# Optimization experiments

Hardware: AMD Instinct MI355X
Metric: run time of the kernel (lower is better)

## Reference

```python
import jax, jax.numpy as jnp
import numpy as np

DIM = 512
HID = 2048
E = 16
B = 8
N = 2048
THRESHOLD = 0.8
CAP_FACTOR = 2.0  # eval mode
MIN_EXPERT_CAPACITY = 4
LOSS_COEF = 0.01
CAP = max(MIN_EXPERT_CAPACITY, min(N, int(N * CAP_FACTOR / E)))  # 256


def setup_inputs() -> dict:
    key = jax.random.key(0)
    k1, k2, k3, k4 = jax.random.split(key, 4)
    x = jax.random.normal(k1, (B, N, DIM), dtype=jnp.float32)
    w_gating = jax.random.normal(k2, (DIM, E), dtype=jnp.float32)
    std1 = 1.0 / np.sqrt(HID)
    std2 = 1.0 / np.sqrt(DIM)
    w1 = jax.random.uniform(k3, (E, DIM, HID), jnp.float32, -std1, std1)
    w2 = jax.random.uniform(k4, (E, HID, DIM), jnp.float32, -std2, std2)
    return {"x": x, "w_gating": w_gating, "w1": w1, "w2": w2}


def _gate(x, w_gating):
    # raw gate probabilities [B, N, E]
    raw = jax.nn.softmax(jnp.einsum('bnd,de->bne', x, w_gating), axis=-1)
    order = jnp.argsort(-raw, axis=-1)                      # descending sort indices
    sp = jnp.take_along_axis(raw, order, axis=-1)           # sorted probs (desc)
    cum = jnp.cumsum(sp, axis=-1)
    tm = cum >= THRESHOLD
    k = jnp.argmax(tm.astype(jnp.float32), axis=-1) + 1     # dynamic k per token
    k = jnp.where(jnp.any(tm, axis=-1), k, E)
    # select top-k in sorted order, renormalize
    rank = jnp.arange(E)
    sel = (rank < k[..., None]).astype(raw.dtype)           # [B,N,E] sorted order
    selp = sp * sel
    normp = selp / jnp.sum(selp, axis=-1, keepdims=True)
    # scatter back to expert order via inverse permutation
    inv = jnp.argsort(order, axis=-1)
    mask = jnp.take_along_axis(sel, inv, axis=-1)           # expert_masks [B,N,E]
    weights = jnp.take_along_axis(normp, inv, axis=-1)      # expert_weights
    # capacity: exclusive cumsum over tokens
    pos = (jnp.cumsum(mask, axis=-2) - mask) * mask
    mask = mask * (pos < float(CAP)).astype(mask.dtype)
    pos = pos * mask
    pos_tok = jnp.sum(pos, axis=-1).astype(jnp.int32)       # [B,N] (summed across experts, as in source)
    in_cap = (pos_tok < CAP).astype(raw.dtype)
    oh = jax.nn.one_hot(pos_tok, CAP, dtype=raw.dtype) * in_cap[..., None]  # [B,N,CAP]
    dispatch = mask[..., None] * oh[..., None, :]           # [B,N,E,CAP]
    combine = (weights * mask)[..., None] * oh[..., None, :]
    density = jnp.mean(mask, axis=-2)
    density_proxy = jnp.mean(raw, axis=-2)
    loss = jnp.mean(density_proxy * density) * float(E * E)
    loss = loss + 0.0 * jnp.mean(k.astype(jnp.float32))
    return dispatch, combine, loss


def reference(x, w_gating, w1, w2):
    dispatch, combine, loss = _gate(x, w_gating)
    expert_inputs = jnp.einsum('bnd,bnec->ebcd', x, dispatch)        # [E,B,CAP,D]
    ei = expert_inputs.reshape(E, B * CAP, DIM)
    hidden = jax.nn.gelu(jnp.einsum('end,edh->enh', ei, w1), approximate=False)
    eo = jnp.einsum('enh,ehd->end', hidden, w2).reshape(E, B, CAP, DIM)
    output = jnp.einsum('ebcd,bnec->bnd', eo, combine)               # [B,N,D]
    return output, loss * LOSS_COEF
```

## Files before the change

### kernel.cpp

```cpp
#include <hip/hip_runtime.h>
#include <math.h>

#define DIMC 512
#define HIDC 2048
#define EC   16
#define BC   8
#define NC   2048
#define CAPC 256
#define BN   (BC * NC)
#define THRESH 0.8f

typedef unsigned short u16;
typedef __attribute__((ext_vector_type(8))) __bf16 bf16x8;
typedef __attribute__((ext_vector_type(4))) float f32x4;

__device__ __forceinline__ float bf2f(unsigned u) {
    union { unsigned i; float f; } v; v.i = u << 16; return v.f;
}
__device__ __forceinline__ u16 f2bf(float f) {
    union { float f; unsigned i; } v; v.f = f;
    unsigned r = v.i + 0x7fff + ((v.i >> 16) & 1);
    return (u16)(r >> 16);
}
__device__ __forceinline__ float gelu_f(float x) {
    float u = 0.7978845608028654f * (x + 0.044715f * x * x * x);
    float t = __expf(2.f * u);
    float th = 1.f - 2.f / (t + 1.f);
    return 0.5f * x * (1.f + th);
}

__global__ void init_kernel(int* __restrict__ heads, int* __restrict__ pos_tok)
{
    int i = blockIdx.x * 256 + threadIdx.x;
    if (i < EC * BC * CAPC) heads[i] = -1;
    if (i < BN) pos_tok[i] = 0;
}

__global__ void wgt_kernel(const float* __restrict__ wg, float* __restrict__ wgt)
{
    int i = blockIdx.x * 256 + threadIdx.x;
    int e = i >> 9, d = i & 511;
    wgt[i] = wg[d * EC + e];
}

__global__ __launch_bounds__(256) void logits_kernel(const float* __restrict__ x,
                                                     const float* __restrict__ wgt,
                                                     float* __restrict__ logits)
{
    int t = threadIdx.x;
    int token = blockIdx.x * 16 + (t >> 4);
    int e = t & 15;
    const float4* xr = (const float4*)(x + (size_t)token * DIMC);
    const float4* wr = (const float4*)(wgt + (size_t)e * DIMC);
    float acc = 0.f;
#pragma unroll 8
    for (int i = 0; i < DIMC / 4; ++i) {
        float4 a = xr[i], b = wr[i];
        acc += a.x * b.x + a.y * b.y + a.z * b.z + a.w * b.w;
    }
    logits[(size_t)token * EC + e] = acc;
}

__global__ __launch_bounds__(256) void gate_epi_kernel(const float* __restrict__ logits,
                                                       float* __restrict__ raw,
                                                       float* __restrict__ weights,
                                                       float* __restrict__ maskf)
{
    int token = blockIdx.x * 256 + threadIdx.x;
    const float4* lp = (const float4*)(logits + (size_t)token * EC);
    float p[EC];
    {
        float4 v0 = lp[0], v1 = lp[1], v2 = lp[2], v3 = lp[3];
        p[0]=v0.x; p[1]=v0.y; p[2]=v0.z; p[3]=v0.w;
        p[4]=v1.x; p[5]=v1.y; p[6]=v1.z; p[7]=v1.w;
        p[8]=v2.x; p[9]=v2.y; p[10]=v2.z; p[11]=v2.w;
        p[12]=v3.x; p[13]=v3.y; p[14]=v3.z; p[15]=v3.w;
    }
    float m = p[0];
#pragma unroll
    for (int e = 1; e < EC; ++e) m = fmaxf(m, p[e]);
    float s = 0.f;
#pragma unroll
    for (int e = 0; e < EC; ++e) { p[e] = expf(p[e] - m); s += p[e]; }
    float inv = 1.f / s;
#pragma unroll
    for (int e = 0; e < EC; ++e) p[e] *= inv;

    int rank[EC]; float cum[EC];
#pragma unroll
    for (int e = 0; e < EC; ++e) {
        int r = 0; float c = p[e];
#pragma unroll
        for (int j = 0; j < EC; ++j) {
            if (j == e) continue;
            bool ahead = (p[j] > p[e]) || (p[j] == p[e] && j < e);
            r += ahead ? 1 : 0;
            c += ahead ? p[j] : 0.f;
        }
        rank[e] = r; cum[e] = c;
    }
    int kr = EC - 1;
#pragma unroll
    for (int e = 0; e < EC; ++e)
        if (cum[e] >= THRESH) kr = min(kr, rank[e]);
    float denom = 0.f;
#pragma unroll
    for (int e = 0; e < EC; ++e) denom += (rank[e] <= kr) ? p[e] : 0.f;
    float invd = 1.f / denom;

    float w[EC], mk[EC];
#pragma unroll
    for (int e = 0; e < EC; ++e) {
        bool sel = rank[e] <= kr;
        w[e]  = sel ? p[e] * invd : 0.f;
        mk[e] = sel ? 1.f : 0.f;
    }
    float4* rp = (float4*)(raw + (size_t)token * EC);
    float4* wp = (float4*)(weights + (size_t)token * EC);
    float4* mp = (float4*)(maskf + (size_t)token * EC);
#pragma unroll
    for (int i = 0; i < 4; ++i) {
        rp[i] = make_float4(p[4*i], p[4*i+1], p[4*i+2], p[4*i+3]);
        wp[i] = make_float4(w[4*i], w[4*i+1], w[4*i+2], w[4*i+3]);
        mp[i] = make_float4(mk[4*i], mk[4*i+1], mk[4*i+2], mk[4*i+3]);
    }
}

__global__ __launch_bounds__(64) void capacity_kernel(const float* __restrict__ raw,
                                                      float* __restrict__ maskf,
                                                      int* __restrict__ pos,
                                                      int* __restrict__ pos_tok,
                                                      float* __restrict__ density,
                                                      float* __restrict__ proxy)
{
    int t = blockIdx.x;
    int b = t / EC, e = t % EC;
    int lane = threadIdx.x;

    int count = 0;
    float rsum = 0.f;
    for (int n0 = 0; n0 < NC; n0 += 64) {
        int n = n0 + lane;
        size_t idx = ((size_t)b * NC + n) * EC + e;
        float mv = maskf[idx];
        rsum += raw[idx];
        unsigned long long bal = __ballot(mv != 0.f);
        int below = __popcll(bal & ((1ull << lane) - 1ull));
        int pval = 0;
        if (mv != 0.f) {
            pval = count + below;
            if (pval >= CAPC) { maskf[idx] = 0.f; pval = 0; }
            else if (pval > 0) atomicAdd(&pos_tok[b * NC + n], pval);
        }
        pos[idx] = pval;
        count += __popcll(bal);
    }
#pragma unroll
    for (int off = 32; off >= 1; off >>= 1) rsum += __shfl_xor(rsum, off);
    if (lane == 0) {
        int admitted = count < CAPC ? count : CAPC;
        density[t] = (float)admitted / (float)NC;
        proxy[t]   = rsum / (float)NC;
    }
}

__global__ __launch_bounds__(256) void build_kernel(const float* __restrict__ maskf,
                                                    const int* __restrict__ pos,
                                                    const int* __restrict__ pos_tok,
                                                    int* __restrict__ heads,
                                                    int* __restrict__ nxt,
                                                    int* __restrict__ node_tok)
{
    int id = blockIdx.x * 256 + threadIdx.x;
    int token = id >> 4, e = id & 15;
    if (maskf[id] == 0.f) return;
    int c = pos_tok[token];
    if (c >= CAPC) return;
    int b = token >> 11;
    int slot = (e * BC + b) * CAPC + c;
    int node = (e * BC + b) * CAPC + pos[id];
    node_tok[node] = token;
    nxt[node] = atomicExch(&heads[slot], node);
}

__global__ __launch_bounds__(256) void gather_ei_kernel(const float* __restrict__ x,
                                                        const int* __restrict__ heads,
                                                        const int* __restrict__ nxt,
                                                        const int* __restrict__ node_tok,
                                                        u16* __restrict__ ei)
{
    int slot = blockIdx.x * 4 + (threadIdx.x >> 6);
    int lane = threadIdx.x & 63;
    float a[8] = {0,0,0,0,0,0,0,0};
    int node = heads[slot];
    while (node >= 0) {
        const float4* xr = (const float4*)(x + (size_t)node_tok[node] * DIMC) + lane * 2;
        float4 v0 = xr[0], v1 = xr[1];
        a[0]+=v0.x; a[1]+=v0.y; a[2]+=v0.z; a[3]+=v0.w;
        a[4]+=v1.x; a[5]+=v1.y; a[6]+=v1.z; a[7]+=v1.w;
        node = nxt[node];
    }
    uint4 v;
    v.x = (unsigned)f2bf(a[0]) | ((unsigned)f2bf(a[1]) << 16);
    v.y = (unsigned)f2bf(a[2]) | ((unsigned)f2bf(a[3]) << 16);
    v.z = (unsigned)f2bf(a[4]) | ((unsigned)f2bf(a[5]) << 16);
    v.w = (unsigned)f2bf(a[6]) | ((unsigned)f2bf(a[7]) << 16);
    *(uint4*)(ei + (size_t)slot * DIMC + lane * 8) = v;
}

__global__ __launch_bounds__(256) void transpose_cvt_kernel(const float* __restrict__ in,
                                                            u16* __restrict__ out,
                                                            int R, int C)
{
    __shared__ float tile[32][33];
    size_t eoff = (size_t)blockIdx.z * R * C;
    const float* ip = in + eoff;
    u16* op = out + eoff;
    int c0 = blockIdx.x * 32, r0 = blockIdx.y * 32;
    int tx = threadIdx.x & 31, ty = threadIdx.x >> 5;
#pragma unroll
    for (int i = 0; i < 32; i += 8)
        tile[ty + i][tx] = ip[(size_t)(r0 + ty + i) * C + c0 + tx];
    __syncthreads();
#pragma unroll
    for (int i = 0; i < 32; i += 8)
        op[(size_t)(c0 + ty + i) * R + r0 + tx] = f2bf(tile[tx][ty + i]);
}

__device__ __forceinline__ void async_cp16(const u16* g, u16* l) {
    __builtin_amdgcn_global_load_lds(
        (const __attribute__((address_space(1))) unsigned*)g,
        (__attribute__((address_space(3))) unsigned*)l, 16, 0, 0);
}

template<int GELU>
__global__ __launch_bounds__(256) void gemm_bt_kernel(
    const u16* __restrict__ A, const u16* __restrict__ Bt, u16* __restrict__ C,
    int M, int N, int K, long sA, long sB, long sC)
{
    __shared__ __align__(16) u16 lds[2][128 * 64];
    int e = blockIdx.z;
    int bm = blockIdx.y * 128, bn = blockIdx.x * 128;
    int t = threadIdx.x, lane = t & 63, w = t >> 6;
    int wm = (w & 1) * 64, wn = (w >> 1) * 64;
    int q = lane >> 4, m16 = lane & 15;

    const u16* gA[4]; const u16* gB[4]; u16 *lA[4], *lB[4];
#pragma unroll
    for (int i = 0; i < 4; ++i) {
        int l = i * 256 + t, r = l >> 3, s = l & 7, c8 = s ^ (r & 7);
        gA[i] = A + (size_t)e * sA + (size_t)(bm + r) * K + c8 * 8;
        gB[i] = Bt + (size_t)e * sB + (size_t)(bn + r) * K + c8 * 8;
        lA[i] = &lds[0][l * 8];
        lB[i] = &lds[1][l * 8];
    }
    int aoff[4][2], boff[4][2];
#pragma unroll
    for (int i = 0; i < 4; ++i) {
        int ra = wm + i * 16 + m16, rb = wn + i * 16 + m16;
#pragma unroll
        for (int h = 0; h < 2; ++h) {
            int c8 = h * 4 + q;
            aoff[i][h] = (ra * 8 + (c8 ^ (ra & 7))) * 8;
            boff[i][h] = (rb * 8 + (c8 ^ (rb & 7))) * 8;
        }
    }

    f32x4 acc[4][4] = {};

    for (int k0 = 0; k0 < K; k0 += 64) {
#pragma unroll
        for (int i = 0; i < 4; ++i) {
            async_cp16(gA[i], lA[i]);
            async_cp16(gB[i], lB[i]);
            gA[i] += 64; gB[i] += 64;
        }
        __syncthreads();
#pragma unroll
        for (int h = 0; h < 2; ++h) {
            bf16x8 af[4], bfr[4];
#pragma unroll
            for (int mt = 0; mt < 4; ++mt) af[mt] = *(const bf16x8*)&lds[0][aoff[mt][h]];
#pragma unroll
            for (int nt = 0; nt < 4; ++nt) bfr[nt] = *(const bf16x8*)&lds[1][boff[nt][h]];
#pragma unroll
            for (int mt = 0; mt < 4; ++mt)
#pragma unroll
                for (int nt = 0; nt < 4; ++nt)
                    acc[mt][nt] = __builtin_amdgcn_mfma_f32_16x16x32_bf16(
                        af[mt], bfr[nt], acc[mt][nt], 0, 0, 0);
        }
        __syncthreads();
    }

    size_t cbase = (size_t)e * sC;
#pragma unroll
    for (int mt = 0; mt < 4; ++mt)
#pragma unroll
        for (int nt = 0; nt < 4; ++nt)
#pragma unroll
            for (int r2 = 0; r2 < 4; ++r2) {
                int row = bm + wm + mt * 16 + q * 4 + r2;
                int col = bn + wn + nt * 16 + m16;
                float v = acc[mt][nt][r2];
                if (GELU) v = gelu_f(v);
                C[cbase + (size_t)row * N + col] = f2bf(v);
            }
}

__global__ __launch_bounds__(256) void combine_kernel(const u16* __restrict__ eo,
                                                      const float* __restrict__ weights,
                                                      const float* __restrict__ maskf,
                                                      const int* __restrict__ pos_tok,
                                                      float* __restrict__ out)
{
    int token = blockIdx.x;
    int tid   = threadIdx.x;
    int b = token >> 11;
    int c = pos_tok[token];
    float a0 = 0.f, a1 = 0.f;
    if (c < CAPC) {
        const float* wr = weights + (size_t)token * EC;
        const float* mr = maskf   + (size_t)token * EC;
#pragma unroll
        for (int e = 0; e < EC; ++e) {
            float wm = wr[e] * mr[e];
            if (wm != 0.f) {
                const u16* src = eo + (((size_t)e * BC + b) * CAPC + c) * DIMC;
                unsigned u = *(const unsigned*)(src + 2 * tid);
                a0 += wm * bf2f(u & 0xffffu);
                a1 += wm * bf2f(u >> 16);
            }
        }
    }
    *(float2*)(out + (size_t)token * DIMC + 2 * tid) = make_float2(a0, a1);
}

__global__ void loss_kernel(const float* __restrict__ density,
                            const float* __restrict__ proxy,
                            float* __restrict__ out_loss)
{
    __shared__ float sh[BC * EC];
    int t = threadIdx.x;
    sh[t] = density[t] * proxy[t];
    __syncthreads();
    for (int s2 = (BC * EC) / 2; s2 >= 1; s2 >>= 1) {
        if (t < s2) sh[t] += sh[t + s2];
        __syncthreads();
    }
    if (t == 0)
        out_loss[0] = sh[0] * ((float)(EC * EC) / (float)(BC * EC)) * 0.01f;
}

extern "C" void kernel_launch(void* const* d_in, const int* in_sizes, int n_in,
                              void* d_out, int out_size, void* d_ws, size_t ws_size,
                              hipStream_t stream)
{
    const float* x  = (const float*)d_in[0];
    const float* wg = (const float*)d_in[1];
    const float* w1 = (const float*)d_in[2];
    const float* w2 = (const float*)d_in[3];
    float* out = (float*)d_out;

    char* ws = (char*)d_ws;
    size_t off = 0;
    auto alloc = [&](size_t bytes) -> void* {
        void* p = ws + off;
        off = (off + bytes + 255) & ~(size_t)255;
        return p;
    };
    float* raw      = (float*)alloc((size_t)BN * EC * 4);
    float* weights  = (float*)alloc((size_t)BN * EC * 4);
    float* maskf    = (float*)alloc((size_t)BN * EC * 4);
    int*   pos      = (int*)  alloc((size_t)BN * EC * 4);
    int*   pos_tok  = (int*)  alloc((size_t)BN * 4);
    int*   heads    = (int*)  alloc((size_t)EC * BC * CAPC * 4);
    int*   nxt      = (int*)  alloc((size_t)EC * BC * CAPC * 4);
    int*   node_tok = (int*)  alloc((size_t)EC * BC * CAPC * 4);
    float* density  = (float*)alloc(BC * EC * 4);
    float* proxy    = (float*)alloc(BC * EC * 4);
    float* logits   = (float*)alloc((size_t)BN * EC * 4);
    float* wgt      = (float*)alloc((size_t)EC * DIMC * 4);
    u16*   ei_bf    = (u16*)alloc((size_t)EC * BC * CAPC * DIMC * 2);
    u16*   w1t      = (u16*)alloc((size_t)EC * DIMC * HIDC * 2);
    u16*   w2t      = (u16*)alloc((size_t)EC * HIDC * DIMC * 2);
    u16*   eo_bf    = (u16*)alloc((size_t)EC * BC * CAPC * DIMC * 2);
    size_t hid_full = (size_t)EC * BC * CAPC * HIDC * 2;
    int ngroups = (ws_size - off >= hid_full) ? 1 : 2;
    int EG = EC / ngroups;
    u16* hidden = (u16*)alloc((size_t)EG * BC * CAPC * HIDC * 2);

    (void)in_sizes; (void)n_in; (void)out_size;

    init_kernel<<<(EC * BC * CAPC + 255) / 256, 256, 0, stream>>>(heads, pos_tok);
    wgt_kernel<<<EC * DIMC / 256, 256, 0, stream>>>(wg, wgt);
    transpose_cvt_kernel<<<dim3(HIDC / 32, DIMC / 32, EC), 256, 0, stream>>>(w1, w1t, DIMC, HIDC);
    transpose_cvt_kernel<<<dim3(DIMC / 32, HIDC / 32, EC), 256, 0, stream>>>(w2, w2t, HIDC, DIMC);

    logits_kernel<<<BN / 16, 256, 0, stream>>>(x, wgt, logits);
    gate_epi_kernel<<<BN / 256, 256, 0, stream>>>(logits, raw, weights, maskf);
    capacity_kernel<<<BC * EC, 64, 0, stream>>>(raw, maskf, pos, pos_tok, density, proxy);
    build_kernel<<<BN * EC / 256, 256, 0, stream>>>(maskf, pos, pos_tok, heads, nxt, node_tok);
    gather_ei_kernel<<<EC * BC * CAPC / 4, 256, 0, stream>>>(x, heads, nxt, node_tok, ei_bf);

    for (int g = 0; g < ngroups; ++g) {
        const u16* Ag  = ei_bf + (size_t)g * EG * BC * CAPC * DIMC;
        const u16* B1g = w1t   + (size_t)g * EG * DIMC * HIDC;
        gemm_bt_kernel<1><<<dim3(HIDC / 128, (BC * CAPC) / 128, EG), 256, 0, stream>>>(
            Ag, B1g, hidden, BC * CAPC, HIDC, DIMC,
            (long)BC * CAPC * DIMC, (long)HIDC * DIMC, (long)BC * CAPC * HIDC);
        const u16* B2g = w2t + (size_t)g * EG * HIDC * DIMC;
        u16* Eg = eo_bf + (size_t)g * EG * BC * CAPC * DIMC;
        gemm_bt_kernel<0><<<dim3(DIMC / 128, (BC * CAPC) / 128, EG), 256, 0, stream>>>(
            hidden, B2g, Eg, BC * CAPC, DIMC, HIDC,
            (long)BC * CAPC * HIDC, (long)DIMC * HIDC, (long)BC * CAPC * DIMC);
    }

    combine_kernel<<<BN, 256, 0, stream>>>(eo_bf, weights, maskf, pos_tok, out);
    loss_kernel<<<1, BC * EC, 0, stream>>>(density, proxy, out + (size_t)BN * DIMC);
}
```

Measured before the change: 527.1 us.

## Fuse gating kernels, double-buffer GEMM LDS, widen transpose tiles, prefetch capacity scan

Merges the logits and gate epilogue kernels into one, passing logits through shared memory so the logits buffer round trip disappears. The expert GEMM now double-buffers its LDS tiles, issuing async copies for the next K-slice before computing the current one, and drops one barrier per iteration. The weight transpose-convert uses 64x64 tiles with float4 loads and 16-byte bf16 stores, and the capacity scan prefetches the next mask and raw values. The gate epilogue now runs on only 16 threads per block, and doubling LDS in the GEMM may reduce occupancy.

```diff
diff --git a/kernel.cpp b/kernel.cpp
--- a/kernel.cpp
+++ b/kernel.cpp
@@ -43,86 +43,85 @@
     wgt[i] = wg[d * EC + e];
 }
 
-__global__ __launch_bounds__(256) void logits_kernel(const float* __restrict__ x,
-                                                     const float* __restrict__ wgt,
-                                                     float* __restrict__ logits)
-{
+__global__ __launch_bounds__(256) void gate_kernel(const float* __restrict__ x,
+                                                   const float* __restrict__ wgt,
+                                                   float* __restrict__ raw,
+                                                   float* __restrict__ weights,
+                                                   float* __restrict__ maskf)
+{
+    __shared__ float lg[16][17];
     int t = threadIdx.x;
-    int token = blockIdx.x * 16 + (t >> 4);
-    int e = t & 15;
-    const float4* xr = (const float4*)(x + (size_t)token * DIMC);
+    int tok16 = t >> 4, e = t & 15;
+    int token0 = blockIdx.x * 16;
+    const float4* xr = (const float4*)(x + (size_t)(token0 + tok16) * DIMC);
     const float4* wr = (const float4*)(wgt + (size_t)e * DIMC);
-    float acc = 0.f;
-#pragma unroll 8
-    for (int i = 0; i < DIMC / 4; ++i) {
-        float4 a = xr[i], b = wr[i];
-        acc += a.x * b.x + a.y * b.y + a.z * b.z + a.w * b.w;
-    }
-    logits[(size_t)token * EC + e] = acc;
-}
-
-__global__ __launch_bounds__(256) void gate_epi_kernel(const float* __restrict__ logits,
-                                                       float* __restrict__ raw,
-                                                       float* __restrict__ weights,
-                                                       float* __restrict__ maskf)
-{
-    int token = blockIdx.x * 256 + threadIdx.x;
-    const float4* lp = (const float4*)(logits + (size_t)token * EC);
-    float p[EC];
-    {
-        float4 v0 = lp[0], v1 = lp[1], v2 = lp[2], v3 = lp[3];
-        p[0]=v0.x; p[1]=v0.y; p[2]=v0.z; p[3]=v0.w;
-        p[4]=v1.x; p[5]=v1.y; p[6]=v1.z; p[7]=v1.w;
-        p[8]=v2.x; p[9]=v2.y; p[10]=v2.z; p[11]=v2.w;
-        p[12]=v3.x; p[13]=v3.y; p[14]=v3.z; p[15]=v3.w;
-    }
-    float m = p[0];
-#pragma unroll
-    for (int e = 1; e < EC; ++e) m = fmaxf(m, p[e]);
-    float s = 0.f;
-#pragma unroll
-    for (int e = 0; e < EC; ++e) { p[e] = expf(p[e] - m); s += p[e]; }
-    float inv = 1.f / s;
-#pragma unroll
-    for (int e = 0; e < EC; ++e) p[e] *= inv;
-
-    int rank[EC]; float cum[EC];
-#pragma unroll
-    for (int e = 0; e < EC; ++e) {
-        int r = 0; float c = p[e];
-#pragma unroll
-        for (int j = 0; j < EC; ++j) {
-            if (j == e) continue;
-            bool ahead = (p[j] > p[e]) || (p[j] == p[e] && j < e);
-            r += ahead ? 1 : 0;
-            c += ahead ? p[j] : 0.f;
-        }
-        rank[e] = r; cum[e] = c;
-    }
-    int kr = EC - 1;
-#pragma unroll
-    for (int e = 0; e < EC; ++e)
-        if (cum[e] >= THRESH) kr = min(kr, rank[e]);
-    float denom = 0.f;
-#pragma unroll
-    for (int e = 0; e < EC; ++e) denom += (rank[e] <= kr) ? p[e] : 0.f;
-    float invd = 1.f / denom;
-
-    float w[EC], mk[EC];
-#pragma unroll
-    for (int e = 0; e < EC; ++e) {
-        bool sel = rank[e] <= kr;
-        w[e]  = sel ? p[e] * invd : 0.f;
-        mk[e] = sel ? 1.f : 0.f;
-    }
-    float4* rp = (float4*)(raw + (size_t)token * EC);
-    float4* wp = (float4*)(weights + (size_t)token * EC);
-    float4* mp = (float4*)(maskf + (size_t)token * EC);
-#pragma unroll
-    for (int i = 0; i < 4; ++i) {
-        rp[i] = make_float4(p[4*i], p[4*i+1], p[4*i+2], p[4*i+3]);
-        wp[i] = make_float4(w[4*i], w[4*i+1], w[4*i+2], w[4*i+3]);
-        mp[i] = make_float4(mk[4*i], mk[4*i+1], mk[4*i+2], mk[4*i+3]);
+
+    float a0 = 0.f, a1 = 0.f, a2 = 0.f, a3 = 0.f;
+#pragma unroll 2
+    for (int i = 0; i < 128; i += 4) {
+        float4 xa = xr[i], xb = xr[i+1], xc = xr[i+2], xd = xr[i+3];
+        float4 wa = wr[i], wb = wr[i+1], wc = wr[i+2], wd = wr[i+3];
+        a0 = fmaf(xa.w, wa.w, fmaf(xa.z, wa.z, fmaf(xa.y, wa.y, fmaf(xa.x, wa.x, a0))));
+        a1 = fmaf(xb.w, wb.w, fmaf(xb.z, wb.z, fmaf(xb.y, wb.y, fmaf(xb.x, wb.x, a1))));
+        a2 = fmaf(xc.w, wc.w, fmaf(xc.z, wc.z, fmaf(xc.y, wc.y, fmaf(xc.x, wc.x, a2))));
+        a3 = fmaf(xd.w, wd.w, fmaf(xd.z, wd.z, fmaf(xd.y, wd.y, fmaf(xd.x, wd.x, a3))));
+    }
+    lg[tok16][e] = (a0 + a1) + (a2 + a3);
+    __syncthreads();
+    if (t < 16) {
+        int token = token0 + t;
+        float p[EC];
+#pragma unroll
+        for (int j = 0; j < EC; ++j) p[j] = lg[t][j];
+
+        float m = p[0];
+#pragma unroll
+        for (int j = 1; j < EC; ++j) m = fmaxf(m, p[j]);
+        float s = 0.f;
+#pragma unroll
+        for (int j = 0; j < EC; ++j) { p[j] = expf(p[j] - m); s += p[j]; }
+        float inv = 1.f / s;
+#pragma unroll
+        for (int j = 0; j < EC; ++j) p[j] *= inv;
+
+        int rank[EC]; float cum[EC];
+#pragma unroll
+        for (int a = 0; a < EC; ++a) {
+            int r = 0; float c = p[a];
+#pragma unroll
+            for (int j = 0; j < EC; ++j) {
+                if (j == a) continue;
+                bool ahead = (p[j] > p[a]) || (p[j] == p[a] && j < a);
+                r += ahead ? 1 : 0;
+                c += ahead ? p[j] : 0.f;
+            }
+            rank[a] = r; cum[a] = c;
+        }
+        int kr = EC - 1;
+#pragma unroll
+        for (int a = 0; a < EC; ++a)
+            if (cum[a] >= THRESH) kr = min(kr, rank[a]);
+        float denom = 0.f;
+#pragma unroll
+        for (int a = 0; a < EC; ++a) denom += (rank[a] <= kr) ? p[a] : 0.f;
+        float invd = 1.f / denom;
+
+        float w[EC], mk[EC];
+#pragma unroll
+        for (int a = 0; a < EC; ++a) {
+            bool sel = rank[a] <= kr;
+            w[a]  = sel ? p[a] * invd : 0.f;
+            mk[a] = sel ? 1.f : 0.f;
+        }
+        float4* rp = (float4*)(raw + (size_t)token * EC);
+        float4* wp = (float4*)(weights + (size_t)token * EC);
+        float4* mp = (float4*)(maskf + (size_t)token * EC);
+#pragma unroll
+        for (int i = 0; i < 4; ++i) {
+            rp[i] = make_float4(p[4*i], p[4*i+1], p[4*i+2], p[4*i+3]);
+            wp[i] = make_float4(w[4*i], w[4*i+1], w[4*i+2], w[4*i+3]);
+            mp[i] = make_float4(mk[4*i], mk[4*i+1], mk[4*i+2], mk[4*i+3]);
+        }
     }
 }
 
@@ -137,23 +136,30 @@
     int b = t / EC, e = t % EC;
     int lane = threadIdx.x;
 
+    size_t idx = ((size_t)b * NC + lane) * EC + e;
+    const size_t step = (size_t)64 * EC;
+    float mv = maskf[idx];
+    float rv = raw[idx];
+
     int count = 0;
     float rsum = 0.f;
     for (int n0 = 0; n0 < NC; n0 += 64) {
-        int n = n0 + lane;
-        size_t idx = ((size_t)b * NC + n) * EC + e;
-        float mv = maskf[idx];
-        rsum += raw[idx];
+        float mn = 0.f, rn = 0.f;
+        if (n0 + 64 < NC) { mn = maskf[idx + step]; rn = raw[idx + step]; }
+
+        rsum += rv;
         unsigned long long bal = __ballot(mv != 0.f);
         int below = __popcll(bal & ((1ull << lane) - 1ull));
         int pval = 0;
         if (mv != 0.f) {
             pval = count + below;
             if (pval >= CAPC) { maskf[idx] = 0.f; pval = 0; }
-            else if (pval > 0) atomicAdd(&pos_tok[b * NC + n], pval);
+            else if (pval > 0) atomicAdd(&pos_tok[b * NC + n0 + lane], pval);
         }
         pos[idx] = pval;
         count += __popcll(bal);
+
+        idx += step; mv = mn; rv = rn;
     }
 #pragma unroll
     for (int off = 32; off >= 1; off >>= 1) rsum += __shfl_xor(rsum, off);
@@ -212,19 +218,29 @@
                                                             u16* __restrict__ out,
                                                             int R, int C)
 {
-    __shared__ float tile[32][33];
+    __shared__ float tile[64][65];
     size_t eoff = (size_t)blockIdx.z * R * C;
-    const float* ip = in + eoff;
-    u16* op = out + eoff;
-    int c0 = blockIdx.x * 32, r0 = blockIdx.y * 32;
-    int tx = threadIdx.x & 31, ty = threadIdx.x >> 5;
-#pragma unroll
-    for (int i = 0; i < 32; i += 8)
-        tile[ty + i][tx] = ip[(size_t)(r0 + ty + i) * C + c0 + tx];
+    int c0 = blockIdx.x * 64, r0 = blockIdx.y * 64;
+    int tid = threadIdx.x;
+    int rr = tid >> 4;
+    int cc = (tid & 15) * 4;
+#pragma unroll
+    for (int i = 0; i < 4; ++i) {
+        float4 v = *(const float4*)(in + eoff + (size_t)(r0 + rr + 16 * i) * C + c0 + cc);
+        tile[rr + 16 * i][cc + 0] = v.x;
+        tile[rr + 16 * i][cc + 1] = v.y;
+        tile[rr + 16 * i][cc + 2] = v.z;
+        tile[rr + 16 * i][cc + 3] = v.w;
+    }
     __syncthreads();
-#pragma unroll
-    for (int i = 0; i < 32; i += 8)
-        op[(size_t)(c0 + ty + i) * R + r0 + tx] = f2bf(tile[tx][ty + i]);
+    int c = tid >> 2;
+    int r8 = (tid & 3) * 16;
+    u16 buf[16];
+#pragma unroll
+    for (int j = 0; j < 16; ++j) buf[j] = f2bf(tile[r8 + j][c]);
+    u16* op = out + eoff + (size_t)(c0 + c) * R + r0 + r8;
+    *(uint4*)(op)     = *(uint4*)&buf[0];
+    *(uint4*)(op + 8) = *(uint4*)&buf[8];
 }
 
 __device__ __forceinline__ void async_cp16(const u16* g, u16* l) {
@@ -238,21 +254,20 @@
     const u16* __restrict__ A, const u16* __restrict__ Bt, u16* __restrict__ C,
     int M, int N, int K, long sA, long sB, long sC)
 {
-    __shared__ __align__(16) u16 lds[2][128 * 64];
+    __shared__ __align__(16) u16 lds[2][2][128 * 64];
     int e = blockIdx.z;
     int bm = blockIdx.y * 128, bn = blockIdx.x * 128;
     int t = threadIdx.x, lane = t & 63, w = t >> 6;
     int wm = (w & 1) * 64, wn = (w >> 1) * 64;
     int q = lane >> 4, m16 = lane & 15;
 
-    const u16* gA[4]; const u16* gB[4]; u16 *lA[4], *lB[4];
+    const u16* gA[4]; const u16* gB[4]; int lofs[4];
 #pragma unroll
     for (int i = 0; i < 4; ++i) {
         int l = i * 256 + t, r = l >> 3, s = l & 7, c8 = s ^ (r & 7);
         gA[i] = A + (size_t)e * sA + (size_t)(bm + r) * K + c8 * 8;
         gB[i] = Bt + (size_t)e * sB + (size_t)(bn + r) * K + c8 * 8;
-        lA[i] = &lds[0][l * 8];
-        lB[i] = &lds[1][l * 8];
+        lofs[i] = l * 8;
     }
     int aoff[4][2], boff[4][2];
 #pragma unroll
@@ -266,23 +281,33 @@
         }
     }
 
+#pragma unroll
+    for (int i = 0; i < 4; ++i) {
+        async_cp16(gA[i], &lds[0][0][lofs[i]]);
+        async_cp16(gB[i], &lds[0][1][lofs[i]]);
+        gA[i] += 64; gB[i] += 64;
+    }
+
     f32x4 acc[4][4] = {};
-
-    for (int k0 = 0; k0 < K; k0 += 64) {
-#pragma unroll
-        for (int i = 0; i < 4; ++i) {
-            async_cp16(gA[i], lA[i]);
-            async_cp16(gB[i], lB[i]);
-            gA[i] += 64; gB[i] += 64;
-        }
+    int nk = K >> 6;
+    for (int ki = 0; ki < nk; ++ki) {
+        int cur = ki & 1, nx = cur ^ 1;
         __syncthreads();
+        if (ki + 1 < nk) {
+#pragma unroll
+            for (int i = 0; i < 4; ++i) {
+                async_cp16(gA[i], &lds[nx][0][lofs[i]]);
+                async_cp16(gB[i], &lds[nx][1][lofs[i]]);
+                gA[i] += 64; gB[i] += 64;
+            }
+        }
 #pragma unroll
         for (int h = 0; h < 2; ++h) {
             bf16x8 af[4], bfr[4];
 #pragma unroll
-            for (int mt = 0; mt < 4; ++mt) af[mt] = *(const bf16x8*)&lds[0][aoff[mt][h]];
-#pragma unroll
-            for (int nt = 0; nt < 4; ++nt) bfr[nt] = *(const bf16x8*)&lds[1][boff[nt][h]];
+            for (int mt = 0; mt < 4; ++mt) af[mt] = *(const bf16x8*)&lds[cur][0][aoff[mt][h]];
+#pragma unroll
+            for (int nt = 0; nt < 4; ++nt) bfr[nt] = *(const bf16x8*)&lds[cur][1][boff[nt][h]];
 #pragma unroll
             for (int mt = 0; mt < 4; ++mt)
 #pragma unroll
@@ -290,7 +315,6 @@
                     acc[mt][nt] = __builtin_amdgcn_mfma_f32_16x16x32_bf16(
                         af[mt], bfr[nt], acc[mt][nt], 0, 0, 0);
         }
-        __syncthreads();
     }
 
     size_t cbase = (size_t)e * sC;
@@ -379,7 +403,6 @@
     int*   node_tok = (int*)  alloc((size_t)EC * BC * CAPC * 4);
     float* density  = (float*)alloc(BC * EC * 4);
     float* proxy    = (float*)alloc(BC * EC * 4);
-    float* logits   = (float*)alloc((size_t)BN * EC * 4);
     float* wgt      = (float*)alloc((size_t)EC * DIMC * 4);
     u16*   ei_bf    = (u16*)alloc((size_t)EC * BC * CAPC * DIMC * 2);
     u16*   w1t      = (u16*)alloc((size_t)EC * DIMC * HIDC * 2);
@@ -394,11 +417,10 @@
 
     init_kernel<<<(EC * BC * CAPC + 255) / 256, 256, 0, stream>>>(heads, pos_tok);
     wgt_kernel<<<EC * DIMC / 256, 256, 0, stream>>>(wg, wgt);
-    transpose_cvt_kernel<<<dim3(HIDC / 32, DIMC / 32, EC), 256, 0, stream>>>(w1, w1t, DIMC, HIDC);
-    transpose_cvt_kernel<<<dim3(DIMC / 32, HIDC / 32, EC), 256, 0, stream>>>(w2, w2t, HIDC, DIMC);
-
-    logits_kernel<<<BN / 16, 256, 0, stream>>>(x, wgt, logits);
-    gate_epi_kernel<<<BN / 256, 256, 0, stream>>>(logits, raw, weights, maskf);
+    transpose_cvt_kernel<<<dim3(HIDC / 64, DIMC / 64, EC), 256, 0, stream>>>(w1, w1t, DIMC, HIDC);
+    transpose_cvt_kernel<<<dim3(DIMC / 64, HIDC / 64, EC), 256, 0, stream>>>(w2, w2t, HIDC, DIMC);
+
+    gate_kernel<<<BN / 16, 256, 0, stream>>>(x, wgt, raw, weights, maskf);
     capacity_kernel<<<BC * EC, 64, 0, stream>>>(raw, maskf, pos, pos_tok, density, proxy);
     build_kernel<<<BN * EC / 256, 256, 0, stream>>>(maskf, pos, pos_tok, heads, nxt, node_tok);
     gather_ei_kernel<<<EC * BC * CAPC / 4, 256, 0, stream>>>(x, heads, nxt, node_tok, ei_bf);
```

After: 518.5 us. No clear change (-1.6%).
